# Kernel optimization log

Hardware: AMD Instinct MI355X
Metric: run time of the kernel (lower is better)

Reference implementation:

```python
import jax, jax.numpy as jnp
from jax import lax
import numpy as np

KSIZE = 7
SIGMA = 5.0
ALPHA = 0.05

def _gaussian_kernel(ksize, sigma):
    ax = np.arange(ksize, dtype=np.float32) - (ksize - 1) / 2.0
    g1 = np.exp(-(ax ** 2) / (2.0 * sigma ** 2))
    k2 = np.outer(g1, g1)
    k2 = k2 / k2.sum()
    return jnp.asarray(k2, dtype=jnp.float32)

def _sobel_kernel():
    sx = np.array([[-1, 0, 1], [-2, 0, 2], [-1, 0, 1]], dtype=np.float32)
    sy = np.array([[-1, -2, -1], [0, 0, 0], [1, 2, 1]], dtype=np.float32)
    return jnp.asarray(np.stack([sx, sy])[:, None], dtype=jnp.float32)  # (2,1,3,3)

def setup_inputs() -> dict:
    key = jax.random.key(0)
    x = jax.random.normal(key, (4, 1, 2048, 2048), dtype=jnp.float32)
    return {"x": x, "sobel_k": _sobel_kernel(), "gauss_k": _gaussian_kernel(KSIZE, SIGMA)}

def reference(x, sobel_k, gauss_k):
    N, _, H, W = x.shape
    dn = ('NCHW', 'OIHW', 'NCHW')
    # Image gradients: Sobel conv, 1 -> 2 channels, same padding
    g = lax.conv_general_dilated(x, sobel_k, (1, 1), [(1, 1), (1, 1)], dimension_numbers=dn)
    Ix, Iy = g[:, 0], g[:, 1]  # (N,H,W)
    # Channel products: I_xx, I_yy, I_xy
    prods = jnp.stack([Ix * Ix, Iy * Iy, Ix * Iy], axis=1)  # (N,3,H,W)
    # Second moment: depthwise 7x7 Gaussian smoothing, same padding
    p = KSIZE // 2
    gk = jnp.broadcast_to(gauss_k[None, None], (3, 1, KSIZE, KSIZE))
    S = lax.conv_general_dilated(prods, gk, (1, 1), [(p, p), (p, p)], dimension_numbers=dn, feature_group_count=3)
    Sxx, Syy, Sxy = S[:, 0], S[:, 1], S[:, 2]
    # Corner response R = det(M) - alpha * trace(M)^2
    R = Sxx * Syy - Sxy * Sxy - ALPHA * (Sxx + Syy) ** 2  # (N,H,W)
    # NMS: global lower-median threshold (torch.median semantics), 7x7 maxpool, equality mask
    n = H * W
    med = jnp.sort(R.reshape(N, -1), axis=1)[:, (n - 1) // 2]  # torch lower median
    Rt = jnp.where(R >= med[:, None, None], R, jnp.float32(0.0))
    mx = lax.reduce_window(Rt, -jnp.inf, lax.max, (1, KSIZE, KSIZE), (1, 1, 1), [(0, 0), (p, p), (p, p)])
    out = jnp.where(Rt == mx, Rt, jnp.float32(0.0))
    return out[:, None]  # (N,1,H,W)
```

## Files before the change

kernel.cpp:

```cpp
#include <hip/hip_runtime.h>

#define H 2048
#define W 2048
#define NIMG 4
#define HWPX (H*W)
#define K_RANK 2097151u

__device__ __forceinline__ unsigned fmap(float f) {
    unsigned u = __float_as_uint(f);
    return (u & 0x80000000u) ? ~u : (u | 0x80000000u);
}

__global__ void k_prep(const float* __restrict__ gk, double* __restrict__ kwd) {
    int t = threadIdx.x;
    if (t < 49) kwd[t] = (double)gk[t];
}

__global__ __launch_bounds__(512, 4) void k_harris_R(const float* __restrict__ x,
                                                     const double* __restrict__ kwd,
                                                     float* __restrict__ R,
                                                     unsigned* __restrict__ hist1)
{
    __align__(16) __shared__ double ixiy[5320];
    __shared__ float xs[2880];
    unsigned* hist = (unsigned*)ixiy;

    const int tid = threadIdx.x;
    const int img = blockIdx.z;
    const int x0 = blockIdx.x * 64, y0 = blockIdx.y * 32;
    const float* __restrict__ X = x + (size_t)img * HWPX;

    for (int i = tid; i < 2880; i += 512) {
        int r = i / 72, c = i - r * 72;
        int gy = y0 - 4 + r, gx = x0 - 4 + c;
        float v = 0.f;
        if ((unsigned)gy < H && (unsigned)gx < W) v = X[(size_t)gy * W + gx];
        xs[i] = v;
    }
    __syncthreads();

    for (int i = tid; i < 2660; i += 512) {
        int r = i / 70, c = i - r * 70;
        double ix = 0.0, iy = 0.0;
        int gy = y0 - 3 + r, gx = x0 - 3 + c;
        if ((unsigned)gy < H && (unsigned)gx < W) {
            const float* p0 = &xs[r * 72 + c];
            double x00 = p0[0],   x01 = p0[1],   x02 = p0[2];
            double x10 = p0[72],                  x12 = p0[74];
            double x20 = p0[144], x21 = p0[145], x22 = p0[146];
            ix = (x02 - x00) + 2.0 * (x12 - x10) + (x22 - x20);
            iy = (x20 - x00) + 2.0 * (x21 - x01) + (x22 - x02);
        }
        ixiy[i] = ix;
        ixiy[2660 + i] = iy;
    }
    __syncthreads();

    const int tc = (tid & 31) * 2;
    const int tr = (tid >> 5) * 2;

    double axx[2][2], ayy[2][2], axy[2][2];
    #pragma unroll
    for (int rr = 0; rr < 2; rr++)
        #pragma unroll
        for (int cc = 0; cc < 2; cc++) { axx[rr][cc] = 0.0; ayy[rr][cc] = 0.0; axy[rr][cc] = 0.0; }

    #pragma unroll
    for (int ii = 0; ii < 8; ii++) {
        const int prow = tr + ii;
        double vx[8], vy[8];
        const double2* rx = (const double2*)&ixiy[prow * 70 + tc];
        const double2* ry = (const double2*)&ixiy[2660 + prow * 70 + tc];
        #pragma unroll
        for (int q = 0; q < 4; q++) {
            double2 t = rx[q]; vx[2*q] = t.x; vx[2*q+1] = t.y;
            double2 u = ry[q]; vy[2*q] = u.x; vy[2*q+1] = u.y;
        }
        double xx0 = vx[0]*vx[0], yy0 = vy[0]*vy[0], xy0 = vx[0]*vy[0];
        #pragma unroll
        for (int j = 0; j < 7; j++) {
            double xx1 = vx[j+1]*vx[j+1], yy1 = vy[j+1]*vy[j+1], xy1 = vx[j+1]*vy[j+1];
            #pragma unroll
            for (int rr = 0; rr < 2; rr++) {
                const int wrow = ii - rr;
                if (wrow >= 0 && wrow <= 6) {
                    double w = kwd[wrow * 7 + j];
                    axx[rr][0] = fma(w, xx0, axx[rr][0]); axx[rr][1] = fma(w, xx1, axx[rr][1]);
                    ayy[rr][0] = fma(w, yy0, ayy[rr][0]); ayy[rr][1] = fma(w, yy1, ayy[rr][1]);
                    axy[rr][0] = fma(w, xy0, axy[rr][0]); axy[rr][1] = fma(w, xy1, axy[rr][1]);
                }
            }
            xx0 = xx1; yy0 = yy1; xy0 = xy1;
        }
    }

    float* __restrict__ Ri = R + (size_t)img * HWPX;
    unsigned bins[4];
    #pragma unroll
    for (int rr = 0; rr < 2; rr++) {
        float2 o;
        #pragma unroll
        for (int cc = 0; cc < 2; cc++) {
            double sxx = axx[rr][cc], syy = ayy[rr][cc], sxy = axy[rr][cc];
            double t2 = sxx + syy;
            double Rv = sxx * syy - sxy * sxy - 0.05 * t2 * t2;
            ((float*)&o)[cc] = (float)Rv;
        }
        *(float2*)&Ri[(size_t)(y0 + tr + rr) * W + (x0 + tc)] = o;
        bins[rr * 2]     = fmap(o.x) >> 20;
        bins[rr * 2 + 1] = fmap(o.y) >> 20;
    }
    __syncthreads();

    for (int i = tid; i < 4096; i += 512) hist[i] = 0;
    __syncthreads();
    #pragma unroll
    for (int q = 0; q < 4; q++) atomicAdd(&hist[bins[q]], 1u);
    __syncthreads();

    unsigned* gh = hist1 + img * 4096;
    for (int i = tid; i < 4096; i += 512) {
        unsigned v = hist[i];
        if (v) atomicAdd(&gh[i], v);
    }
}

__global__ __launch_bounds__(256) void k_scan1(const unsigned* __restrict__ hist1,
                                               int* __restrict__ metaBin,
                                               int* __restrict__ metaBase)
{
    int img = blockIdx.x, tid = threadIdx.x;
    __shared__ unsigned s[256];
    const unsigned* h = hist1 + img * 4096;
    unsigned loc[16], sum = 0;
    #pragma unroll
    for (int j = 0; j < 16; j++) { loc[j] = h[tid * 16 + j]; sum += loc[j]; }
    s[tid] = sum; __syncthreads();
    for (int off = 1; off < 256; off <<= 1) {
        unsigned v = (tid >= off) ? s[tid - off] : 0; __syncthreads();
        s[tid] += v; __syncthreads();
    }
    unsigned incl = s[tid], excl = incl - sum;
    if (K_RANK >= excl && K_RANK < incl) {
        unsigned run = excl;
        #pragma unroll
        for (int j = 0; j < 16; j++) {
            if (K_RANK < run + loc[j]) { metaBin[img] = tid * 16 + j; metaBase[img] = (int)run; break; }
            run += loc[j];
        }
    }
}

__global__ __launch_bounds__(256) void k_hist2(const float* __restrict__ R,
                                               const int* __restrict__ metaBin,
                                               unsigned* __restrict__ hist2)
{
    int img = blockIdx.x >> 10;
    unsigned b1 = (unsigned)metaBin[img];
    unsigned* h2 = hist2 + ((size_t)img << 20);
    const float4* __restrict__ R4 = (const float4*)R + (size_t)blockIdx.x * 1024;
    #pragma unroll
    for (int j = 0; j < 4; j++) {
        float4 v = R4[threadIdx.x + j * 256];
        unsigned ux = fmap(v.x), uy = fmap(v.y), uz = fmap(v.z), uw = fmap(v.w);
        if ((ux >> 20) == b1) atomicAdd(&h2[ux & 0xFFFFFu], 1u);
        if ((uy >> 20) == b1) atomicAdd(&h2[uy & 0xFFFFFu], 1u);
        if ((uz >> 20) == b1) atomicAdd(&h2[uz & 0xFFFFFu], 1u);
        if ((uw >> 20) == b1) atomicAdd(&h2[uw & 0xFFFFFu], 1u);
    }
}

__global__ __launch_bounds__(256) void k_med(const unsigned* __restrict__ hist2,
                                             unsigned* __restrict__ chunkSum,
                                             const int* __restrict__ metaBin,
                                             const int* __restrict__ metaBase,
                                             float* __restrict__ med,
                                             unsigned* __restrict__ ticket2)
{
    __shared__ unsigned s[256];
    __shared__ unsigned lastv;
    __shared__ int sel[2];
    const int tid = threadIdx.x;
    const int cb = blockIdx.x, img = blockIdx.y;

    const unsigned* h = hist2 + ((size_t)img << 20) + cb * 4096;
    unsigned sum = 0;
    #pragma unroll
    for (int j = 0; j < 16; j++) sum += h[tid + j * 256];
    s[tid] = sum; __syncthreads();
    for (int off = 128; off > 0; off >>= 1) {
        if (tid < off) s[tid] += s[tid + off];
        __syncthreads();
    }
    if (tid == 0) {
        atomicExch(&chunkSum[img * 256 + cb], s[0]);
        __threadfence();
        lastv = atomicAdd(ticket2, 1u);
    }
    __syncthreads();
    if (lastv != NIMG * 256 - 1) return;

    for (int im = 0; im < NIMG; im++) {
        unsigned target = K_RANK - (unsigned)metaBase[im];
        unsigned v = atomicAdd(&chunkSum[im * 256 + tid], 0u);
        __syncthreads();
        s[tid] = v; __syncthreads();
        for (int off = 1; off < 256; off <<= 1) {
            unsigned t2 = (tid >= off) ? s[tid - off] : 0; __syncthreads();
            s[tid] += t2; __syncthreads();
        }
        unsigned incl = s[tid], excl = incl - v;
        if (target >= excl && target < incl) { sel[0] = tid; sel[1] = (int)excl; }
        __syncthreads();
        int scb = sel[0];
        unsigned cexcl = (unsigned)sel[1];

        const unsigned* hh = hist2 + ((size_t)im << 20) + scb * 4096;
        unsigned loc[16], lsum = 0;
        #pragma unroll
        for (int j = 0; j < 16; j++) { loc[j] = hh[tid * 16 + j]; lsum += loc[j]; }
        __syncthreads();
        s[tid] = lsum; __syncthreads();
        for (int off = 1; off < 256; off <<= 1) {
            unsigned t2 = (tid >= off) ? s[tid - off] : 0; __syncthreads();
            s[tid] += t2; __syncthreads();
        }
        incl = s[tid] + cexcl; excl = s[tid] - lsum + cexcl;
        if (target >= excl && target < incl) {
            unsigned run = excl;
            #pragma unroll
            for (int j = 0; j < 16; j++) {
                if (target < run + loc[j]) {
                    unsigned c = (unsigned)scb * 4096u + (unsigned)tid * 16u + (unsigned)j;
                    unsigned mu = (((unsigned)metaBin[im]) << 20) | c;
                    unsigned fb = (mu & 0x80000000u) ? (mu & 0x7FFFFFFFu) : ~mu;
                    med[im] = __uint_as_float(fb);
                    break;
                }
                run += loc[j];
            }
        }
        __syncthreads();
    }
}

__global__ __launch_bounds__(256) void k_out(const float* __restrict__ R,
                                             const float* __restrict__ med,
                                             float* __restrict__ out)
{
    __shared__ float rt[38][39];
    __shared__ float hm[38][33];
    const int tid = threadIdx.x;
    const int img = blockIdx.z;
    const int x0 = blockIdx.x * 32, y0 = blockIdx.y * 32;
    const float m = med[img];
    const float* __restrict__ Ri = R + ((size_t)img << 22);

    for (int i = tid; i < 1444; i += 256) {
        int r = i / 38, c = i - r * 38;
        int gy = y0 - 3 + r, gx = x0 - 3 + c;
        float v = -INFINITY;
        if ((unsigned)gy < H && (unsigned)gx < W) {
            float rv = Ri[(size_t)gy * W + gx];
            v = (rv >= m) ? rv : 0.0f;
        }
        rt[r][c] = v;
    }
    __syncthreads();

    for (int i = tid; i < 1216; i += 256) {
        int r = i >> 5, c = i & 31;
        float mx = rt[r][c];
        #pragma unroll
        for (int j = 1; j < 7; j++) mx = fmaxf(mx, rt[r][c + j]);
        hm[r][c] = mx;
    }
    __syncthreads();

    const int txc = tid & 31, ty0 = tid >> 5;
    float* __restrict__ Oi = out + ((size_t)img << 22);
    #pragma unroll
    for (int q = 0; q < 4; q++) {
        int ty = ty0 + q * 8;
        float mx = hm[ty][txc];
        #pragma unroll
        for (int j = 1; j < 7; j++) mx = fmaxf(mx, hm[ty + j][txc]);
        float c = rt[ty + 3][txc + 3];
        Oi[(size_t)(y0 + ty) * W + (x0 + txc)] = (c == mx) ? c : 0.0f;
    }
}

extern "C" void kernel_launch(void* const* d_in, const int* in_sizes, int n_in,
                              void* d_out, int out_size, void* d_ws, size_t ws_size,
                              hipStream_t stream)
{
    const float* x  = (const float*)d_in[0];
    const float* gk = (const float*)d_in[2];
    float* out = (float*)d_out;

    char* ws = (char*)d_ws;
    float*    R        = (float*)ws;
    unsigned* hist1    = (unsigned*)(ws + (size_t)HWPX * NIMG * 4);
    unsigned* ticket1  = hist1 + NIMG * 4096;
    unsigned* ticket2  = ticket1 + 4;
    unsigned* chunkSum = ticket2 + 1;
    int*      metaBin  = (int*)(chunkSum + 1024);
    int*      metaBase = metaBin + NIMG;
    float*    med      = (float*)(metaBase + NIMG);
    double*   kwd      = (double*)(ws + (size_t)HWPX * NIMG * 4 + 71680);
    unsigned* hist2    = (unsigned*)d_out;

    hipMemsetAsync(hist1, 0, (size_t)NIMG * 4096 * 4 + 32, stream);
    hipMemsetAsync(hist2, 0, (size_t)NIMG * (1u << 20) * 4, stream);

    k_prep    <<<1, 64, 0, stream>>>(gk, kwd);
    k_harris_R<<<dim3(32, 64, NIMG), 512, 0, stream>>>(x, kwd, R, hist1);
    k_scan1   <<<NIMG, 256, 0, stream>>>(hist1, metaBin, metaBase);
    k_hist2   <<<4096, 256, 0, stream>>>(R, metaBin, hist2);
    k_med     <<<dim3(256, NIMG), 256, 0, stream>>>(hist2, chunkSum, metaBin, metaBase, med, ticket2);
    k_out     <<<dim3(64, 64, NIMG), 256, 0, stream>>>(R, med, out);
}
```

Measured before the change: 304.9 us.

## Fold histogram zeroing into kernels and shrink input tile shared memory

Replaces the two hipMemsetAsync calls by zeroing hist1 inside k_prep and hist2 inside k_harris_R, each block clearing its own slice. The input tile in shared memory is reduced from 40 to 24 rows and loaded in two passes, so the gradient computation runs in two phases with ring-indexed rows. The intent is to drop two memset launches and cut LDS use per block to allow more resident blocks, at the cost of extra syncthreads and index arithmetic.

```diff
diff --git a/kernel.cpp b/kernel.cpp
--- a/kernel.cpp
+++ b/kernel.cpp
@@ -11,18 +11,24 @@
     return (u & 0x80000000u) ? ~u : (u | 0x80000000u);
 }
 
-__global__ void k_prep(const float* __restrict__ gk, double* __restrict__ kwd) {
-    int t = threadIdx.x;
+__global__ __launch_bounds__(512) void k_prep(const float* __restrict__ gk,
+                                              double* __restrict__ kwd,
+                                              unsigned* __restrict__ hist1z)
+{
+    int t = blockIdx.x * 512 + threadIdx.x;
     if (t < 49) kwd[t] = (double)gk[t];
+    hist1z[t] = 0u;
+    if (t < 8) hist1z[16384 + t] = 0u;
 }
 
 __global__ __launch_bounds__(512, 4) void k_harris_R(const float* __restrict__ x,
                                                      const double* __restrict__ kwd,
                                                      float* __restrict__ R,
-                                                     unsigned* __restrict__ hist1)
+                                                     unsigned* __restrict__ hist1,
+                                                     unsigned* __restrict__ hist2z)
 {
     __align__(16) __shared__ double ixiy[5320];
-    __shared__ float xs[2880];
+    __shared__ float xs[1728];
     unsigned* hist = (unsigned*)ixiy;
 
     const int tid = threadIdx.x;
@@ -30,7 +36,12 @@
     const int x0 = blockIdx.x * 64, y0 = blockIdx.y * 32;
     const float* __restrict__ X = x + (size_t)img * HWPX;
 
-    for (int i = tid; i < 2880; i += 512) {
+    {
+        int bidlin = ((img * gridDim.y) + blockIdx.y) * gridDim.x + blockIdx.x;
+        hist2z[(size_t)bidlin * 512 + tid] = 0u;
+    }
+
+    for (int i = tid; i < 1728; i += 512) {
         int r = i / 72, c = i - r * 72;
         int gy = y0 - 4 + r, gx = x0 - 4 + c;
         float v = 0.f;
@@ -39,7 +50,7 @@
     }
     __syncthreads();
 
-    for (int i = tid; i < 2660; i += 512) {
+    for (int i = tid; i < 1540; i += 512) {
         int r = i / 70, c = i - r * 70;
         double ix = 0.0, iy = 0.0;
         int gy = y0 - 3 + r, gx = x0 - 3 + c;
@@ -51,8 +62,39 @@
             ix = (x02 - x00) + 2.0 * (x12 - x10) + (x22 - x20);
             iy = (x20 - x00) + 2.0 * (x21 - x01) + (x22 - x02);
         }
-        ixiy[i] = ix;
-        ixiy[2660 + i] = iy;
+        ixiy[r * 70 + c] = ix;
+        ixiy[2660 + r * 70 + c] = iy;
+    }
+    __syncthreads();
+
+    for (int i = tid; i < 1152; i += 512) {
+        int r24 = i / 72, c = i - r24 * 72;
+        int gy = y0 + 20 + r24, gx = x0 - 4 + c;
+        float v = 0.f;
+        if ((unsigned)gy < H && (unsigned)gx < W) v = X[(size_t)gy * W + gx];
+        xs[i] = v;
+    }
+    __syncthreads();
+
+    for (int i = tid; i < 1120; i += 512) {
+        int r = 22 + i / 70, c = i - (r - 22) * 70;
+        double ix = 0.0, iy = 0.0;
+        int gy = y0 - 3 + r, gx = x0 - 3 + c;
+        if ((unsigned)gy < H && (unsigned)gx < W) {
+            int s0 = (r     < 24) ? r     : r - 24;
+            int s1 = (r + 1 < 24) ? r + 1 : r - 23;
+            int s2 = (r + 2 < 24) ? r + 2 : r - 22;
+            const float* q0 = &xs[s0 * 72 + c];
+            const float* q1 = &xs[s1 * 72 + c];
+            const float* q2 = &xs[s2 * 72 + c];
+            double x00 = q0[0], x01 = q0[1], x02 = q0[2];
+            double x10 = q1[0],               x12 = q1[2];
+            double x20 = q2[0], x21 = q2[1], x22 = q2[2];
+            ix = (x02 - x00) + 2.0 * (x12 - x10) + (x22 - x20);
+            iy = (x20 - x00) + 2.0 * (x21 - x01) + (x22 - x02);
+        }
+        ixiy[r * 70 + c] = ix;
+        ixiy[2660 + r * 70 + c] = iy;
     }
     __syncthreads();
 
@@ -310,11 +352,8 @@
     double*   kwd      = (double*)(ws + (size_t)HWPX * NIMG * 4 + 71680);
     unsigned* hist2    = (unsigned*)d_out;
 
-    hipMemsetAsync(hist1, 0, (size_t)NIMG * 4096 * 4 + 32, stream);
-    hipMemsetAsync(hist2, 0, (size_t)NIMG * (1u << 20) * 4, stream);
-
-    k_prep    <<<1, 64, 0, stream>>>(gk, kwd);
-    k_harris_R<<<dim3(32, 64, NIMG), 512, 0, stream>>>(x, kwd, R, hist1);
+    k_prep    <<<32, 512, 0, stream>>>(gk, kwd, hist1);
+    k_harris_R<<<dim3(32, 64, NIMG), 512, 0, stream>>>(x, kwd, R, hist1, hist2);
     k_scan1   <<<NIMG, 256, 0, stream>>>(hist1, metaBin, metaBase);
     k_hist2   <<<4096, 256, 0, stream>>>(R, metaBin, hist2);
     k_med     <<<dim3(256, NIMG), 256, 0, stream>>>(hist2, chunkSum, metaBin, metaBase, med, ticket2);
```

Result: slower. 317.1 us (+4.0%).
